# Kernel tuning notes

Measured on AMD Instinct MI355X. Metric: run time of the kernel, lower is better.

Reference implementation:

```python
import jax, jax.numpy as jnp
import numpy as np

NUM_UNITS = 512
NUM_IN = 256
BATCH = 8192


def _to_complex(x):
    # torch.view_as_complex on x.view(B, N, 2): even cols real, odd cols imag
    x2 = x.reshape(x.shape[0], -1, 2)
    return jax.lax.complex(x2[..., 0], x2[..., 1])


def _diag_mul(w, z):
    return (jnp.cos(w) + 1j * jnp.sin(w)) * z


def _reflect(re, im, z):
    v = jax.lax.complex(re, im)                      # [N]
    vstar_z = jnp.sum(jnp.conj(v) * z, axis=1, keepdims=True)  # [B,1]
    sq_norm = jnp.sum(re * re + im * im)
    return z - (2.0 / sq_norm) * vstar_z * v


def _modrelu(z, bias):
    norm = jnp.abs(z)
    scale = jax.nn.relu(norm + bias) / (norm + 1e-6)
    return scale * z


def setup_inputs() -> dict:
    key = jax.random.key(0)
    ks = jax.random.split(key, 12)
    two_pi = 2.0 * np.pi
    inputs = jax.random.normal(ks[0], (BATCH, NUM_IN), dtype=jnp.float32)
    states = jax.random.normal(ks[1], (BATCH, 2 * NUM_UNITS), dtype=jnp.float32)
    # xavier_uniform for w_ih [2N, num_in]
    bound = np.sqrt(6.0 / (2 * NUM_UNITS + NUM_IN)).astype(np.float32)
    w_ih = jax.random.uniform(ks[2], (2 * NUM_UNITS, NUM_IN), jnp.float32, -bound, bound)
    b_h = jnp.zeros((NUM_UNITS,), jnp.float32)
    d1_w = jax.random.uniform(ks[3], (NUM_UNITS,), jnp.float32, -np.pi, np.pi)
    d2_w = jax.random.uniform(ks[4], (NUM_UNITS,), jnp.float32, -np.pi, np.pi)
    d3_w = jax.random.uniform(ks[5], (NUM_UNITS,), jnp.float32, -np.pi, np.pi)
    r1_re = jax.random.uniform(ks[6], (NUM_UNITS,), jnp.float32, -1.0, 1.0)
    r1_im = jax.random.uniform(ks[7], (NUM_UNITS,), jnp.float32, -1.0, 1.0)
    r2_re = jax.random.uniform(ks[8], (NUM_UNITS,), jnp.float32, -1.0, 1.0)
    r2_im = jax.random.uniform(ks[9], (NUM_UNITS,), jnp.float32, -1.0, 1.0)
    perm = jax.random.permutation(ks[10], NUM_UNITS).astype(jnp.int64)
    return {"inputs": inputs, "states": states, "w_ih": w_ih, "b_h": b_h,
            "d1_w": d1_w, "r1_re": r1_re, "r1_im": r1_im, "perm": perm,
            "d2_w": d2_w, "r2_re": r2_re, "r2_im": r2_im, "d3_w": d3_w}


def reference(inputs, states, w_ih, b_h, d1_w, r1_re, r1_im, perm,
              d2_w, r2_re, r2_im, d3_w):
    inputs_mul = inputs @ w_ih.T                      # [B, 2N]
    inputs_mul_c = _to_complex(inputs_mul)            # [B, N] complex
    state_c = _to_complex(states)                     # [B, N] complex

    z = _diag_mul(d1_w, state_c)
    z = jnp.fft.fft(z, axis=1)
    z = _reflect(r1_re, r1_im, z)
    z = z[:, perm]
    z = _diag_mul(d2_w, z)
    z = jnp.fft.ifft(z, axis=1)
    z = _reflect(r2_re, r2_im, z)
    z = _diag_mul(d3_w, z)

    preact = inputs_mul_c + z
    new_c = _modrelu(preact, b_h)
    return jnp.concatenate([new_c.real, new_c.imag], axis=1)  # [B, 2N]
```

## Files before the change

### kernel.cpp

```cpp
#include <hip/hip_runtime.h>
#include <math.h>

#define BATCH 8192
#define NU 512
#define NIN 256

typedef __attribute__((ext_vector_type(8))) __bf16 bf16x8;
typedef __attribute__((ext_vector_type(4))) float f32x4;

__device__ __forceinline__ float2 cmul(float2 a, float2 b){
    return make_float2(a.x*b.x - a.y*b.y, a.x*b.y + a.y*b.x);
}

__device__ __forceinline__ unsigned int pack2bf(float x, float y){
    unsigned int ux = __float_as_uint(x);
    ux = (ux + 0x7FFFu + ((ux >> 16) & 1u)) >> 16;
    unsigned int uy = __float_as_uint(y);
    uy = (uy + 0x7FFFu + ((uy >> 16) & 1u)) & 0xFFFF0000u;
    return ux | uy;
}


__device__ __forceinline__ void stage_tile(const float* __restrict__ G,
                                           char* __restrict__ lds,
                                           int kb, int tid){
    const int r0 = tid >> 3;
    const int kc = (tid & 7) << 3;
    #pragma unroll
    for (int it = 0; it < 4; ++it){
        const int row = r0 + (it << 5);
        const float* g = G + (size_t)row * NIN + kb + kc;
        float4 v0 = *(const float4*)g;
        float4 v1 = *(const float4*)(g + 4);
        int4 w;
        w.x = (int)pack2bf(v0.x, v0.y);
        w.y = (int)pack2bf(v0.z, v0.w);
        w.z = (int)pack2bf(v1.x, v1.y);
        w.w = (int)pack2bf(v1.z, v1.w);
        int off = (row << 7) + (kc << 1);
        off ^= (row & 7) << 4;
        *(int4*)(lds + off) = w;
    }
}

__global__ __launch_bounds__(256) void gemm_bf16(const float* __restrict__ A,
                                                 const float* __restrict__ W,
                                                 float* __restrict__ P){
    __shared__ __align__(16) char As[128*64*2];
    __shared__ __align__(16) char Bs[128*64*2];
    const int tid  = threadIdx.x;
    const int lane = tid & 63, wv = tid >> 6;
    const int wm = wv >> 1, wn = wv & 1;
    const int bm = blockIdx.y, bn = blockIdx.x;

    const float* Ag = A + (size_t)bm * 128 * NIN;
    const float* Wg = W + (size_t)bn * 128 * NIN;

    f32x4 acc[4][4] = {};
    const int frow = lane & 15;
    const int kq   = (lane >> 4) << 4;

    for (int kb = 0; kb < NIN; kb += 64){
        if (kb) __syncthreads();
        stage_tile(Ag, As, kb, tid);
        stage_tile(Wg, Bs, kb, tid);
        __syncthreads();
        #pragma unroll
        for (int ks = 0; ks < 2; ++ks){
            const int koff = kq + (ks << 6);
            bf16x8 a[4], b[4];
            #pragma unroll
            for (int i = 0; i < 4; ++i){
                const int ar = wm*64 + i*16 + frow;
                a[i] = *(const bf16x8*)(As + (((ar << 7) + koff) ^ ((ar & 7) << 4)));
                const int br = wn*64 + i*16 + frow;
                b[i] = *(const bf16x8*)(Bs + (((br << 7) + koff) ^ ((br & 7) << 4)));
            }
            #pragma unroll
            for (int mi = 0; mi < 4; ++mi)
                #pragma unroll
                for (int ni = 0; ni < 4; ++ni)
                    acc[mi][ni] = __builtin_amdgcn_mfma_f32_16x16x32_bf16(
                        a[mi], b[ni], acc[mi][ni], 0, 0, 0);
        }
    }
    const int prow0 = bm*128 + wm*64 + ((lane >> 4) << 2);
    const int pcol0 = bn*128 + wn*64 + frow;
    #pragma unroll
    for (int mi = 0; mi < 4; ++mi)
        #pragma unroll
        for (int ni = 0; ni < 4; ++ni)
            #pragma unroll
            for (int r = 0; r < 4; ++r)
                P[(size_t)(prow0 + mi*16 + r) * 1024 + pcol0 + ni*16] = acc[mi][ni][r];
}


template<int CONJ>
__device__ __forceinline__ void fft512(float2* buf, const float2* twid, int t){
    #pragma unroll
    for (int s = 1; s <= 9; ++s){
        int half = 1 << (s-1);
        int j  = t & (half-1);
        int i1 = ((t >> (s-1)) << s) + j;
        int i2 = i1 + half;
        float2 w = twid[j << (9-s)];
        if (CONJ) w.y = -w.y;
        float2 a  = buf[i1];
        float2 bb = cmul(w, buf[i2]);
        buf[i1] = make_float2(a.x+bb.x, a.y+bb.y);
        buf[i2] = make_float2(a.x-bb.x, a.y-bb.y);
        __syncthreads();
    }
}

__device__ __forceinline__ void reflect(float2* buf, const float* __restrict__ vre,
                                        const float* __restrict__ vim,
                                        float* red, int t){
    float2 z0 = buf[t], z1 = buf[t+256];
    float2 v0 = make_float2(vre[t],     vim[t]);
    float2 v1 = make_float2(vre[t+256], vim[t+256]);
    float pr = v0.x*z0.x + v0.y*z0.y + v1.x*z1.x + v1.y*z1.y;
    float pi = v0.x*z0.y - v0.y*z0.x + v1.x*z1.y - v1.y*z1.x;
    float nn = v0.x*v0.x + v0.y*v0.y + v1.x*v1.x + v1.y*v1.y;
    #pragma unroll
    for (int off = 32; off > 0; off >>= 1){
        pr += __shfl_down(pr, off);
        pi += __shfl_down(pi, off);
        nn += __shfl_down(nn, off);
    }
    int wave = t >> 6;
    if ((t & 63) == 0){ red[wave*3+0] = pr; red[wave*3+1] = pi; red[wave*3+2] = nn; }
    __syncthreads();
    pr = red[0] + red[3] + red[6] + red[9];
    pi = red[1] + red[4] + red[7] + red[10];
    nn = red[2] + red[5] + red[8] + red[11];
    float coef = 2.0f / nn;
    float2 c = make_float2(coef*pr, coef*pi);
    float2 d0 = cmul(c, v0), d1v = cmul(c, v1);
    buf[t]     = make_float2(z0.x - d0.x,  z0.y - d0.y);
    buf[t+256] = make_float2(z1.x - d1v.x, z1.y - d1v.y);
    __syncthreads();
}

__global__ __launch_bounds__(256) void urnn_kernel(
        const float* __restrict__ states,
        const float* __restrict__ b_h,
        const float* __restrict__ d1_w,
        const float* __restrict__ r1_re, const float* __restrict__ r1_im,
        const int* __restrict__ perm,
        const float* __restrict__ d2_w,
        const float* __restrict__ r2_re, const float* __restrict__ r2_im,
        const float* __restrict__ d3_w,
        float* __restrict__ out )
{
    __shared__ float2 bufA[512];
    __shared__ float2 bufB[512];
    __shared__ float2 twid[256];
    __shared__ float  red[12];
    const int t = threadIdx.x;
    const int b = blockIdx.x;

    {
        float ang = -6.283185307179586f * (float)t / 512.0f;
        float sn, cs; __sincosf(ang, &sn, &cs);
        twid[t] = make_float2(cs, sn);
    }

    {
        float4 s4 = ((const float4*)(states + (size_t)b*1024))[t];
        float2 dw = ((const float2*)d1_w)[t];
        float sn, cs;
        __sincosf(dw.x, &sn, &cs);
        float2 z0 = cmul(make_float2(cs, sn), make_float2(s4.x, s4.y));
        __sincosf(dw.y, &sn, &cs);
        float2 z1 = cmul(make_float2(cs, sn), make_float2(s4.z, s4.w));
        bufA[__brev(2*t)   >> 23] = z0;
        bufA[__brev(2*t+1) >> 23] = z1;
    }
    __syncthreads();

    fft512<0>(bufA, twid, t);
    reflect(bufA, r1_re, r1_im, red, t);

    #pragma unroll
    for (int q = 0; q < 2; ++q){
        int i = t + q*256;
        int src = perm[i];
        float2 zv = bufA[src];
        float sn, cs; __sincosf(d2_w[i], &sn, &cs);
        zv = cmul(make_float2(cs, sn), zv);
        bufB[__brev(i) >> 23] = zv;
    }
    __syncthreads();

    fft512<1>(bufB, twid, t);
    reflect(bufB, r2_re, r2_im, red, t);

    float* orow = out + (size_t)b*1024;
    const float inv = 1.0f/512.0f;
    float2 res0, res1;
    {
        float2 c0 = ((const float2*)orow)[t];
        float2 z0 = bufB[t];
        float sn, cs; __sincosf(d3_w[t], &sn, &cs);
        float2 zz = cmul(make_float2(cs, sn), z0);
        float2 pre = make_float2(c0.x + zz.x*inv, c0.y + zz.y*inv);
        float norm = sqrtf(pre.x*pre.x + pre.y*pre.y);
        float sc = fmaxf(norm + b_h[t], 0.0f) / (norm + 1e-6f);
        res0 = make_float2(sc*pre.x, sc*pre.y);
    }
    {
        float2 c1 = ((const float2*)orow)[t+256];
        float2 z1 = bufB[t+256];
        float sn, cs; __sincosf(d3_w[t+256], &sn, &cs);
        float2 zz = cmul(make_float2(cs, sn), z1);
        float2 pre = make_float2(c1.x + zz.x*inv, c1.y + zz.y*inv);
        float norm = sqrtf(pre.x*pre.x + pre.y*pre.y);
        float sc = fmaxf(norm + b_h[t+256], 0.0f) / (norm + 1e-6f);
        res1 = make_float2(sc*pre.x, sc*pre.y);
    }
    __syncthreads();
    orow[t]       = res0.x;
    orow[t+512]   = res0.y;
    orow[t+256]   = res1.x;
    orow[t+768]   = res1.y;
}

extern "C" void kernel_launch(void* const* d_in, const int* in_sizes, int n_in,
                              void* d_out, int out_size, void* d_ws, size_t ws_size,
                              hipStream_t stream) {
    const float* inputs = (const float*)d_in[0];
    const float* states = (const float*)d_in[1];
    const float* w_ih   = (const float*)d_in[2];
    const float* b_h    = (const float*)d_in[3];
    const float* d1_w   = (const float*)d_in[4];
    const float* r1_re  = (const float*)d_in[5];
    const float* r1_im  = (const float*)d_in[6];
    const int*   perm   = (const int*)d_in[7];
    const float* d2_w   = (const float*)d_in[8];
    const float* r2_re  = (const float*)d_in[9];
    const float* r2_im  = (const float*)d_in[10];
    const float* d3_w   = (const float*)d_in[11];
    float* out = (float*)d_out;

    dim3 gA(8, 64);
    gemm_bf16<<<gA, 256, 0, stream>>>(inputs, w_ih, out);
    urnn_kernel<<<BATCH, 256, 0, stream>>>(states, b_h, d1_w, r1_re, r1_im,
                                           perm, d2_w, r2_re, r2_im, d3_w, out);
}
```

Before: 187.1 us.

## Compute each row's FFT in one wavefront with registers and shuffles

The per-row kernel now maps one batch row to one 64-lane wavefront, holding 8 complex values per lane. Both 512-point FFTs run as register butterflies plus cross-lane shuffles, and the bit-reversal, permutation and phase tables are precomputed once per block in LDS. This removes the nine block-wide barriers per FFT and most LDS traffic. The GEMM epilogue is also restaged through LDS so the outputs go out as coalesced float4 stores. In exchange, twiddles are recomputed with sincos in registers and register pressure rises.

```diff
diff --git a/kernel.cpp b/kernel.cpp
--- a/kernel.cpp
+++ b/kernel.cpp
@@ -10,6 +10,15 @@
 
 __device__ __forceinline__ float2 cmul(float2 a, float2 b){
     return make_float2(a.x*b.x - a.y*b.y, a.x*b.y + a.y*b.x);
+}
+__device__ __forceinline__ float2 cadd(float2 a, float2 b){ return make_float2(a.x+b.x, a.y+b.y); }
+__device__ __forceinline__ float2 csub(float2 a, float2 b){ return make_float2(a.x-b.x, a.y-b.y); }
+
+template<bool INV>
+__device__ __forceinline__ float2 twid512(int idx){
+    float ang = 0.012271846303085129f * (float)idx;
+    float sn, cs; __sincosf(INV ? ang : -ang, &sn, &cs);
+    return make_float2(cs, sn);
 }
 
 __device__ __forceinline__ unsigned int pack2bf(float x, float y){
@@ -46,8 +55,9 @@
 __global__ __launch_bounds__(256) void gemm_bf16(const float* __restrict__ A,
                                                  const float* __restrict__ W,
                                                  float* __restrict__ P){
-    __shared__ __align__(16) char As[128*64*2];
-    __shared__ __align__(16) char Bs[128*64*2];
+    __shared__ __align__(16) char smem[2 * 128*64*2];
+    char* As = smem;
+    char* Bs = smem + 128*64*2;
     const int tid  = threadIdx.x;
     const int lane = tid & 63, wv = tid >> 6;
     const int wm = wv >> 1, wn = wv & 1;
@@ -84,66 +94,148 @@
                         a[mi], b[ni], acc[mi][ni], 0, 0, 0);
         }
     }
-    const int prow0 = bm*128 + wm*64 + ((lane >> 4) << 2);
-    const int pcol0 = bn*128 + wn*64 + frow;
-    #pragma unroll
-    for (int mi = 0; mi < 4; ++mi)
-        #pragma unroll
-        for (int ni = 0; ni < 4; ++ni)
+
+    float* stg = (float*)smem;
+    const int lr4 = (lane >> 4) << 2;
+    #pragma unroll
+    for (int q = 0; q < 4; ++q){
+        __syncthreads();
+        if (wm == (q >> 1)){
+            const int miBase = (q & 1) * 2;
             #pragma unroll
-            for (int r = 0; r < 4; ++r)
-                P[(size_t)(prow0 + mi*16 + r) * 1024 + pcol0 + ni*16] = acc[mi][ni][r];
-}
-
-
-template<int CONJ>
-__device__ __forceinline__ void fft512(float2* buf, const float2* twid, int t){
-    #pragma unroll
-    for (int s = 1; s <= 9; ++s){
-        int half = 1 << (s-1);
-        int j  = t & (half-1);
-        int i1 = ((t >> (s-1)) << s) + j;
-        int i2 = i1 + half;
-        float2 w = twid[j << (9-s)];
-        if (CONJ) w.y = -w.y;
-        float2 a  = buf[i1];
-        float2 bb = cmul(w, buf[i2]);
-        buf[i1] = make_float2(a.x+bb.x, a.y+bb.y);
-        buf[i2] = make_float2(a.x-bb.x, a.y-bb.y);
+            for (int mj = 0; mj < 2; ++mj)
+                #pragma unroll
+                for (int ni = 0; ni < 4; ++ni)
+                    #pragma unroll
+                    for (int r = 0; r < 4; ++r)
+                        stg[(lr4 + mj*16 + r)*132 + wn*64 + ni*16 + frow]
+                            = acc[miBase + mj][ni][r];
+        }
         __syncthreads();
-    }
-}
-
-__device__ __forceinline__ void reflect(float2* buf, const float* __restrict__ vre,
-                                        const float* __restrict__ vim,
-                                        float* red, int t){
-    float2 z0 = buf[t], z1 = buf[t+256];
-    float2 v0 = make_float2(vre[t],     vim[t]);
-    float2 v1 = make_float2(vre[t+256], vim[t+256]);
-    float pr = v0.x*z0.x + v0.y*z0.y + v1.x*z1.x + v1.y*z1.y;
-    float pi = v0.x*z0.y - v0.y*z0.x + v1.x*z1.y - v1.y*z1.x;
-    float nn = v0.x*v0.x + v0.y*v0.y + v1.x*v1.x + v1.y*v1.y;
+        #pragma unroll
+        for (int it = 0; it < 4; ++it){
+            int idx = it*256 + tid;
+            int r32 = idx >> 5;
+            int c4  = idx & 31;
+            float4 v = *(const float4*)(stg + r32*132 + c4*4);
+            int grow = bm*128 + (q >> 1)*64 + (q & 1)*32 + r32;
+            *(float4*)(P + (size_t)grow*1024 + bn*128 + c4*4) = v;
+        }
+    }
+}
+
+
+__device__ __forceinline__ void fft_fwd(float2 z[8], int l){
+    #pragma unroll
+    for (int r = 0; r < 4; ++r){
+        float2 w = twid512<false>(r*64 + l);
+        float2 a = z[r], b = z[r+4];
+        z[r]   = cadd(a, b);
+        z[r+4] = cmul(w, csub(a, b));
+    }
+    {
+        float2 w0 = twid512<false>(2*l), w1 = twid512<false>(2*(64+l));
+        const int gs[4] = {0,1,4,5};
+        #pragma unroll
+        for (int k = 0; k < 4; ++k){
+            int g = gs[k];
+            float2 w = (g & 1) ? w1 : w0;
+            float2 a = z[g], b = z[g+2];
+            z[g]   = cadd(a, b);
+            z[g+2] = cmul(w, csub(a, b));
+        }
+    }
+    {
+        float2 w = twid512<false>(4*l);
+        #pragma unroll
+        for (int g = 0; g < 8; g += 2){
+            float2 a = z[g], b = z[g+1];
+            z[g]   = cadd(a, b);
+            z[g+1] = cmul(w, csub(a, b));
+        }
+    }
+    #pragma unroll
+    for (int h = 32; h >= 1; h >>= 1){
+        int m = 256 / h;
+        float2 w = twid512<false>(m * (l & (h-1)));
+        bool low = (l & h) != 0;
+        #pragma unroll
+        for (int r = 0; r < 8; ++r){
+            float2 p;
+            p.x = __shfl_xor(z[r].x, h);
+            p.y = __shfl_xor(z[r].y, h);
+            z[r] = low ? cmul(w, csub(p, z[r])) : cadd(z[r], p);
+        }
+    }
+}
+
+__device__ __forceinline__ void fft_inv(float2 z[8], int l){
+    #pragma unroll
+    for (int h = 1; h <= 32; h <<= 1){
+        int m = 256 / h;
+        float2 w = twid512<true>(m * (l & (h-1)));
+        bool low = (l & h) != 0;
+        #pragma unroll
+        for (int r = 0; r < 8; ++r){
+            float2 p;
+            p.x = __shfl_xor(z[r].x, h);
+            p.y = __shfl_xor(z[r].y, h);
+            float2 t = cmul(w, low ? z[r] : p);
+            z[r] = low ? csub(p, t) : cadd(z[r], t);
+        }
+    }
+    {
+        float2 w = twid512<true>(4*l);
+        #pragma unroll
+        for (int g = 0; g < 8; g += 2){
+            float2 b = cmul(w, z[g+1]);
+            z[g+1] = csub(z[g], b);
+            z[g]   = cadd(z[g], b);
+        }
+    }
+    {
+        float2 w0 = twid512<true>(2*l), w1 = twid512<true>(2*(64+l));
+        const int gs[4] = {0,1,4,5};
+        #pragma unroll
+        for (int k = 0; k < 4; ++k){
+            int g = gs[k];
+            float2 w = (g & 1) ? w1 : w0;
+            float2 b = cmul(w, z[g+2]);
+            z[g+2] = csub(z[g], b);
+            z[g]   = cadd(z[g], b);
+        }
+    }
+    #pragma unroll
+    for (int r = 0; r < 4; ++r){
+        float2 w = twid512<true>(r*64 + l);
+        float2 b = cmul(w, z[r+4]);
+        z[r+4] = csub(z[r], b);
+        z[r]   = cadd(z[r], b);
+    }
+}
+
+__device__ __forceinline__ void wave_reflect(float2 z[8], const float2 v[8]){
+    float pr = 0.f, pi = 0.f, nn = 0.f;
+    #pragma unroll
+    for (int r = 0; r < 8; ++r){
+        pr += v[r].x*z[r].x + v[r].y*z[r].y;
+        pi += v[r].x*z[r].y - v[r].y*z[r].x;
+        nn += v[r].x*v[r].x + v[r].y*v[r].y;
+    }
     #pragma unroll
     for (int off = 32; off > 0; off >>= 1){
-        pr += __shfl_down(pr, off);
-        pi += __shfl_down(pi, off);
-        nn += __shfl_down(nn, off);
-    }
-    int wave = t >> 6;
-    if ((t & 63) == 0){ red[wave*3+0] = pr; red[wave*3+1] = pi; red[wave*3+2] = nn; }
-    __syncthreads();
-    pr = red[0] + red[3] + red[6] + red[9];
-    pi = red[1] + red[4] + red[7] + red[10];
-    nn = red[2] + red[5] + red[8] + red[11];
-    float coef = 2.0f / nn;
-    float2 c = make_float2(coef*pr, coef*pi);
-    float2 d0 = cmul(c, v0), d1v = cmul(c, v1);
-    buf[t]     = make_float2(z0.x - d0.x,  z0.y - d0.y);
-    buf[t+256] = make_float2(z1.x - d1v.x, z1.y - d1v.y);
-    __syncthreads();
-}
-
-__global__ __launch_bounds__(256) void urnn_kernel(
+        pr += __shfl_xor(pr, off);
+        pi += __shfl_xor(pi, off);
+        nn += __shfl_xor(nn, off);
+    }
+    float c2 = 2.0f / nn;
+    float2 cc = make_float2(c2*pr, c2*pi);
+    #pragma unroll
+    for (int r = 0; r < 8; ++r)
+        z[r] = csub(z[r], cmul(cc, v[r]));
+}
+
+__global__ __launch_bounds__(256) void urnn_wave(
         const float* __restrict__ states,
         const float* __restrict__ b_h,
         const float* __restrict__ d1_w,
@@ -154,77 +246,87 @@
         const float* __restrict__ d3_w,
         float* __restrict__ out )
 {
-    __shared__ float2 bufA[512];
-    __shared__ float2 bufB[512];
-    __shared__ float2 twid[256];
-    __shared__ float  red[12];
-    const int t = threadIdx.x;
-    const int b = blockIdx.x;
-
-    {
-        float ang = -6.283185307179586f * (float)t / 512.0f;
-        float sn, cs; __sincosf(ang, &sn, &cs);
-        twid[t] = make_float2(cs, sn);
-    }
-
-    {
-        float4 s4 = ((const float4*)(states + (size_t)b*1024))[t];
-        float2 dw = ((const float2*)d1_w)[t];
-        float sn, cs;
-        __sincosf(dw.x, &sn, &cs);
-        float2 z0 = cmul(make_float2(cs, sn), make_float2(s4.x, s4.y));
-        __sincosf(dw.y, &sn, &cs);
-        float2 z1 = cmul(make_float2(cs, sn), make_float2(s4.z, s4.w));
-        bufA[__brev(2*t)   >> 23] = z0;
-        bufA[__brev(2*t+1) >> 23] = z1;
+    __shared__ float2 zbuf[4][512];
+    __shared__ float2 vb1[512];
+    __shared__ float2 t2[512];
+    __shared__ unsigned short gidx[512];
+
+    const int tid = threadIdx.x;
+    const int l = tid & 63, wv = tid >> 6;
+
+    #pragma unroll
+    for (int q = 0; q < 2; ++q){
+        int s = tid + q*256;
+        int i = __brev((unsigned)s) >> 23;
+        vb1[s] = make_float2(r1_re[i], r1_im[i]);
+        float sn, cs; __sincosf(d2_w[i], &sn, &cs);
+        t2[s] = make_float2(cs, sn);
+        gidx[s] = (unsigned short)(__brev((unsigned)perm[i]) >> 23);
     }
     __syncthreads();
 
-    fft512<0>(bufA, twid, t);
-    reflect(bufA, r1_re, r1_im, red, t);
-
-    #pragma unroll
-    for (int q = 0; q < 2; ++q){
-        int i = t + q*256;
-        int src = perm[i];
-        float2 zv = bufA[src];
-        float sn, cs; __sincosf(d2_w[i], &sn, &cs);
-        zv = cmul(make_float2(cs, sn), zv);
-        bufB[__brev(i) >> 23] = zv;
-    }
-    __syncthreads();
-
-    fft512<1>(bufB, twid, t);
-    reflect(bufB, r2_re, r2_im, red, t);
-
-    float* orow = out + (size_t)b*1024;
+    const int row = blockIdx.x * 4 + wv;
+    const float* srow = states + (size_t)row * 1024;
+    float* orow = out + (size_t)row * 1024;
+
+    float2 c[8];
+    #pragma unroll
+    for (int r = 0; r < 8; ++r) c[r] = ((const float2*)orow)[r*64 + l];
+
+    float2 z[8];
+    #pragma unroll
+    for (int r = 0; r < 8; ++r){
+        int e = r*64 + l;
+        float2 st = ((const float2*)srow)[e];
+        float sn, cs; __sincosf(d1_w[e], &sn, &cs);
+        z[r] = cmul(make_float2(cs, sn), st);
+    }
+
+    fft_fwd(z, l);
+
+    {
+        float2 v[8];
+        #pragma unroll
+        for (int r = 0; r < 8; ++r) v[r] = vb1[r*64 + l];
+        wave_reflect(z, v);
+    }
+
+    {
+        float2* zw = zbuf[wv];
+        #pragma unroll
+        for (int r = 0; r < 8; ++r) zw[r*64 + l] = z[r];
+        __syncthreads();
+        #pragma unroll
+        for (int r = 0; r < 8; ++r){
+            int s = r*64 + l;
+            z[r] = cmul(t2[s], zw[gidx[s]]);
+        }
+    }
+
+    fft_inv(z, l);
+
+    {
+        float2 v[8];
+        #pragma unroll
+        for (int r = 0; r < 8; ++r){
+            int e = r*64 + l;
+            v[r] = make_float2(r2_re[e], r2_im[e]);
+        }
+        wave_reflect(z, v);
+    }
+
     const float inv = 1.0f/512.0f;
-    float2 res0, res1;
-    {
-        float2 c0 = ((const float2*)orow)[t];
-        float2 z0 = bufB[t];
-        float sn, cs; __sincosf(d3_w[t], &sn, &cs);
-        float2 zz = cmul(make_float2(cs, sn), z0);
-        float2 pre = make_float2(c0.x + zz.x*inv, c0.y + zz.y*inv);
-        float norm = sqrtf(pre.x*pre.x + pre.y*pre.y);
-        float sc = fmaxf(norm + b_h[t], 0.0f) / (norm + 1e-6f);
-        res0 = make_float2(sc*pre.x, sc*pre.y);
-    }
-    {
-        float2 c1 = ((const float2*)orow)[t+256];
-        float2 z1 = bufB[t+256];
-        float sn, cs; __sincosf(d3_w[t+256], &sn, &cs);
-        float2 zz = cmul(make_float2(cs, sn), z1);
-        float2 pre = make_float2(c1.x + zz.x*inv, c1.y + zz.y*inv);
-        float norm = sqrtf(pre.x*pre.x + pre.y*pre.y);
-        float sc = fmaxf(norm + b_h[t+256], 0.0f) / (norm + 1e-6f);
-        res1 = make_float2(sc*pre.x, sc*pre.y);
-    }
-    __syncthreads();
-    orow[t]       = res0.x;
-    orow[t+512]   = res0.y;
-    orow[t+256]   = res1.x;
-    orow[t+768]   = res1.y;
+    #pragma unroll
+    for (int r = 0; r < 8; ++r){
+        int e = r*64 + l;
+        float sn, cs; __sincosf(d3_w[e], &sn, &cs);
+        float2 zz = cmul(make_float2(cs, sn), z[r]);
+        float2 pre = make_float2(c[r].x + zz.x*inv, c[r].y + zz.y*inv);
+        float nrm = sqrtf(pre.x*pre.x + pre.y*pre.y);
+        float sc = fmaxf(nrm + b_h[e], 0.f) / (nrm + 1e-6f);
+        orow[e]       = sc*pre.x;
+        orow[e + 512] = sc*pre.y;
+    }
 }
 
 extern "C" void kernel_launch(void* const* d_in, const int* in_sizes, int n_in,
@@ -246,6 +348,6 @@
 
     dim3 gA(8, 64);
     gemm_bf16<<<gA, 256, 0, stream>>>(inputs, w_ih, out);
-    urnn_kernel<<<BATCH, 256, 0, stream>>>(states, b_h, d1_w, r1_re, r1_im,
+    urnn_wave<<<BATCH/4, 256, 0, stream>>>(states, b_h, d1_w, r1_re, r1_im,
                                            perm, d2_w, r2_re, r2_im, d3_w, out);
 }
```

Result: faster. 159.8 us (-14.6%).
